# Performance work log

Measured on AMD Instinct MI355X. Metric: run time of the kernel, lower is better.

The kernel has to match this reference:

```python
import jax, jax.numpy as jnp
import numpy as np

BOHR = 1.8897261258369282  # Angstrom -> Bohr, as in SKparam
CUTOFF = 6.0
LATTICE = np.diag([5.0, 5.0, 5.0]).astype(np.float32)
N_ATOMS, N_SPECIES, N_POLY, N_KPT = 512, 4, 12, 32


def _compute_shifts():
    # Exact replica of DFTB.compute_shift in numpy.
    inv = np.linalg.inv(LATTICE)
    n_rep = np.ceil(np.linalg.norm(inv, axis=0) * CUTOFF).astype(int)
    grid = np.stack(np.meshgrid(*[np.arange(-n, n + 1) for n in n_rep], indexing='ij'), -1).reshape(-1, 3)
    a = np.where(grid > 0, grid - 1, grid)
    shrunk = np.where(a < 0, grid + 1, a)              # shrink each component toward 0 by 1
    sh2 = shrunk.astype(np.float32) @ LATTICE           # lattice.T @ r == r @ lattice
    keep = np.linalg.norm(sh2, axis=1) < CUTOFF
    return (grid[keep].astype(np.float32) @ LATTICE)    # [S,3], S=81 for this lattice/cutoff


def setup_inputs() -> dict:
    key = jax.random.key(0)
    k1, k2, k3, k4, k5 = jax.random.split(key, 5)
    positions = jax.random.uniform(k1, (N_ATOMS, 3), dtype=jnp.float32) * 5.0
    species = jax.random.randint(k2, (N_ATOMS,), 0, N_SPECIES)
    kpoints = jax.random.uniform(k3, (N_KPT, 3), dtype=jnp.float32)
    # decaying per-degree scale keeps polyval bounded at x = cutoff*BOHR ~ 11.3
    scale = (1.0 / 12.0) ** jnp.arange(N_POLY, dtype=jnp.float32)
    param_matrix = jax.random.normal(k4, (N_SPECIES, N_SPECIES, N_POLY), dtype=jnp.float32) * scale
    onsite = jax.random.normal(k5, (N_SPECIES,), dtype=jnp.float32)
    shifts = jnp.asarray(_compute_shifts())
    return {"positions": positions, "species": species, "kpoints": kpoints,
            "param_matrix": param_matrix, "onsite": onsite, "shifts": shifts}


def reference(positions, species, kpoints, param_matrix, onsite, shifts):
    # pairwise distance vectors under periodic shifts: [N,N,S,3]
    dvec = positions[None, :, None, :] + shifts[None, None, :, :] - positions[:, :, None][:, None].reshape(-1, 1, 1, 3)
    dvec = positions[None, :, None, :] + shifts[None, None, :, :] - positions[:, None, None, :]
    dr2 = jnp.sum(dvec * dvec, axis=-1)                       # [N,N,S]
    dr = jnp.sqrt(jnp.where(dr2 > 0.0, dr2, 1.0))
    dr = jnp.where(dr2 > 0.0, dr, 0.0)
    x = dr * BOHR
    # species-pair gather of Vsss polynomial coefficients: [N,N,P]
    coeffs = param_matrix[species[:, None], species[None, :]]
    # Horner eval (torch polyval: p[0] is the constant term after fliplr)
    y = jnp.zeros_like(x)
    for k in range(N_POLY - 1, -1, -1):
        y = y * x + coeffs[:, :, k][:, :, None]
    # calc_tb_params mask: zero for onsite (dr<=0.1) and beyond cutoff
    V = jnp.where((dr > 0.1) & (dr <= CUTOFF), y, 0.0)        # [N,N,S]
    # Bloch phases per k-point and shift (calc_phase_matrix, vectorized)
    inv_lat = jnp.asarray(np.linalg.inv(LATTICE))
    kc = kpoints @ inv_lat.T                                   # [K,3]
    ang = (2.0 * np.pi) * (kc @ shifts.T)                      # [K,S]
    Hr = jnp.einsum('ijs,ks->kij', V, jnp.cos(ang))            # [K,N,N]
    Hi = jnp.einsum('ijs,ks->kij', V, jnp.sin(ang))
    Hr = Hr + jnp.diag(onsite[species])[None]                  # onsite diagonal
    return jnp.stack([Hr, Hi])                                 # [2,K,N,N] real view of complex H
```

## Files before the change

### kernel.cpp

```cpp
#include <hip/hip_runtime.h>

#define NATOMS 512
#define NKPT 32
#define NPOLY 12
#define NSMAX 96
#define NSP 4
#define TI 4
#define TJ 64
#define NTHREADS 256

__global__ __launch_bounds__(NTHREADS, 4)
void dftb_kernel(const float* __restrict__ positions,
                 const int* __restrict__ species,
                 const float* __restrict__ kpoints,
                 const float* __restrict__ param,
                 const float* __restrict__ onsite,
                 const float* __restrict__ shifts,
                 float* __restrict__ out,
                 int ns)
{
    __shared__ float tab[NSMAX][64];
    __shared__ float4 sh4[NSMAX];
    __shared__ float cpar[NSP*NSP*NPOLY];
    __shared__ float4 pjs[TJ];
    __shared__ float4 pis[TI];
    __shared__ int sjs[TJ];
    __shared__ int sis[TI];

    const int tid = threadIdx.x;
    const int bi = blockIdx.x >> 3;
    const int bj = blockIdx.x & 7;

    if (ns > NSMAX) ns = NSMAX;

    for (int idx = tid; idx < ns; idx += NTHREADS)
        sh4[idx] = make_float4(shifts[idx*3+0], shifts[idx*3+1], shifts[idx*3+2], 0.0f);
    for (int idx = tid; idx < NSP*NSP*NPOLY; idx += NTHREADS)
        cpar[idx] = param[idx];
    if (tid < TJ) {
        int j = bj*TJ + tid;
        pjs[tid] = make_float4(positions[j*3+0], positions[j*3+1], positions[j*3+2], 0.0f);
        sjs[tid] = species[j];
    } else if (tid < TJ + TI) {
        int r = tid - TJ;
        int i = bi*TI + r;
        pis[r] = make_float4(positions[i*3+0], positions[i*3+1], positions[i*3+2], 0.0f);
        sis[r] = species[i];
    }
    for (int idx = tid; idx < ns*NKPT; idx += NTHREADS) {
        int s = idx >> 5;
        int k = idx & 31;
        float kcx = kpoints[k*3+0] * 0.2f;
        float kcy = kpoints[k*3+1] * 0.2f;
        float kcz = kpoints[k*3+2] * 0.2f;
        float d = (kcx*shifts[s*3+0] + kcy*shifts[s*3+1]) + kcz*shifts[s*3+2];
        float ang = 6.283185307179586f * d;
        float sn, cs;
        sincosf(ang, &sn, &cs);
        tab[s][k]      = cs;
        tab[s][32 + k] = sn;
    }
    __syncthreads();

    const int li = tid >> 6;
    const int lj = tid & 63;
    const int i = bi*TI + li;
    const int j = bj*TJ + lj;
    const float4 pi4 = pis[li];
    const float4 pj4 = pjs[lj];
    const int si = sis[li];
    const int sj = sjs[lj];

    float c[NPOLY];
    #pragma unroll
    for (int q = 0; q < NPOLY; ++q) c[q] = cpar[(si*NSP + sj)*NPOLY + q];

    float accR[NKPT], accI[NKPT];
    #pragma unroll
    for (int k = 0; k < NKPT; ++k) { accR[k] = 0.0f; accI[k] = 0.0f; }

    for (int s = 0; s < ns; ++s) {
        const float4 sh = sh4[s];
        float dx = (pj4.x + sh.x) - pi4.x;
        float dy = (pj4.y + sh.y) - pi4.y;
        float dz = (pj4.z + sh.z) - pi4.z;
        float dr2 = (__fmul_rn(dx,dx) + __fmul_rn(dy,dy)) + __fmul_rn(dz,dz);
        float dr = sqrtf(dr2);
        bool ok = (dr > 0.1f) && (dr <= 6.0f);
        if (__ballot(ok) == 0ULL) continue;
        float x = dr * 1.8897261258369282f;
        float y = c[NPOLY-1];
        #pragma unroll
        for (int q = NPOLY-2; q >= 0; --q) y = fmaf(y, x, c[q]);
        float V = ok ? y : 0.0f;
        const float4* tp = (const float4*)(&tab[s][0]);
        #pragma unroll
        for (int q = 0; q < 8; ++q) {
            float4 cv = tp[q];
            accR[4*q+0] = fmaf(V, cv.x, accR[4*q+0]);
            accR[4*q+1] = fmaf(V, cv.y, accR[4*q+1]);
            accR[4*q+2] = fmaf(V, cv.z, accR[4*q+2]);
            accR[4*q+3] = fmaf(V, cv.w, accR[4*q+3]);
        }
        #pragma unroll
        for (int q = 0; q < 8; ++q) {
            float4 sv = tp[8+q];
            accI[4*q+0] = fmaf(V, sv.x, accI[4*q+0]);
            accI[4*q+1] = fmaf(V, sv.y, accI[4*q+1]);
            accI[4*q+2] = fmaf(V, sv.z, accI[4*q+2]);
            accI[4*q+3] = fmaf(V, sv.w, accI[4*q+3]);
        }
    }

    const float oi = (i == j) ? onsite[si] : 0.0f;
    float* outR = out + (size_t)i*NATOMS + j;
    float* outI = outR + (size_t)NKPT*NATOMS*NATOMS;
    #pragma unroll
    for (int k = 0; k < NKPT; ++k) {
        outR[(size_t)k*NATOMS*NATOMS] = accR[k] + oi;
        outI[(size_t)k*NATOMS*NATOMS] = accI[k];
    }
}

extern "C" void kernel_launch(void* const* d_in, const int* in_sizes, int n_in,
                              void* d_out, int out_size, void* d_ws, size_t ws_size,
                              hipStream_t stream) {
    const float* positions = (const float*)d_in[0];
    const int*   species   = (const int*)d_in[1];
    const float* kpoints   = (const float*)d_in[2];
    const float* param     = (const float*)d_in[3];
    const float* onsite    = (const float*)d_in[4];
    const float* shifts    = (const float*)d_in[5];
    int ns = in_sizes[5] / 3;
    float* out = (float*)d_out;

    dim3 grid((NATOMS/TI) * (NATOMS/TJ));
    dftb_kernel<<<grid, NTHREADS, 0, stream>>>(positions, species, kpoints,
                                               param, onsite, shifts, out, ns);
}
```

Before: 40.66 us.

## Compute shift-phase contraction with bf16 MFMA via shared-memory V and phase tiles

Restructures the kernel into two phases. First, each thread evaluates the masked polynomial V for all shifts and stores it as bf16 in shared memory, alongside a bf16 cos/sin phase table. Then each wave runs 16x16x32 bf16 MFMA instructions to contract V against the phase table, writing float4 rows per k-point with onsite added on the diagonal. This moves the dominant FMA contraction off the vector ALUs onto matrix cores, at the cost of bf16 rounding of V and the phases and of larger shared-memory use that lowers occupancy.

```diff
diff --git a/kernel.cpp b/kernel.cpp
--- a/kernel.cpp
+++ b/kernel.cpp
@@ -1,124 +1,135 @@
 #include <hip/hip_runtime.h>
 
 #define NATOMS 512
+#define N2 (NATOMS*NATOMS)
 #define NKPT 32
 #define NPOLY 12
+#define NSP 4
 #define NSMAX 96
-#define NSP 4
+#define KSTR 104
 #define TI 4
 #define TJ 64
 #define NTHREADS 256
 
-__global__ __launch_bounds__(NTHREADS, 4)
-void dftb_kernel(const float* __restrict__ positions,
-                 const int* __restrict__ species,
-                 const float* __restrict__ kpoints,
-                 const float* __restrict__ param,
-                 const float* __restrict__ onsite,
-                 const float* __restrict__ shifts,
-                 float* __restrict__ out,
-                 int ns)
+typedef __attribute__((ext_vector_type(8))) short bf16x8;
+typedef __attribute__((ext_vector_type(4))) float f32x4;
+
+static __device__ __forceinline__ unsigned short f2bf(float f) {
+    union { float f; unsigned u; } x; x.f = f;
+    unsigned r = x.u + 0x7FFFu + ((x.u >> 16) & 1u);
+    return (unsigned short)(r >> 16);
+}
+
+__global__ __launch_bounds__(NTHREADS, 2)
+void dftb_mfma(const float* __restrict__ positions,
+               const int* __restrict__ species,
+               const float* __restrict__ kpoints,
+               const float* __restrict__ param,
+               const float* __restrict__ onsite,
+               const float* __restrict__ shifts,
+               float* __restrict__ out, int ns)
 {
-    __shared__ float tab[NSMAX][64];
+    __shared__ unsigned short Vt[NTHREADS][KSTR];
+    __shared__ unsigned short Tt[64][KSTR];
     __shared__ float4 sh4[NSMAX];
     __shared__ float cpar[NSP*NSP*NPOLY];
-    __shared__ float4 pjs[TJ];
-    __shared__ float4 pis[TI];
-    __shared__ int sjs[TJ];
-    __shared__ int sis[TI];
 
     const int tid = threadIdx.x;
     const int bi = blockIdx.x >> 3;
     const int bj = blockIdx.x & 7;
-
     if (ns > NSMAX) ns = NSMAX;
 
-    for (int idx = tid; idx < ns; idx += NTHREADS)
-        sh4[idx] = make_float4(shifts[idx*3+0], shifts[idx*3+1], shifts[idx*3+2], 0.0f);
+    for (int idx = tid; idx < 64*(KSTR/2); idx += NTHREADS)
+        ((unsigned*)Tt)[idx] = 0u;
+    for (int idx = tid; idx < NSMAX; idx += NTHREADS) {
+        if (idx < ns) sh4[idx] = make_float4(shifts[idx*3], shifts[idx*3+1], shifts[idx*3+2], 0.f);
+        else          sh4[idx] = make_float4(0.f, 0.f, 0.f, 0.f);
+    }
     for (int idx = tid; idx < NSP*NSP*NPOLY; idx += NTHREADS)
         cpar[idx] = param[idx];
-    if (tid < TJ) {
-        int j = bj*TJ + tid;
-        pjs[tid] = make_float4(positions[j*3+0], positions[j*3+1], positions[j*3+2], 0.0f);
-        sjs[tid] = species[j];
-    } else if (tid < TJ + TI) {
-        int r = tid - TJ;
-        int i = bi*TI + r;
-        pis[r] = make_float4(positions[i*3+0], positions[i*3+1], positions[i*3+2], 0.0f);
-        sis[r] = species[i];
+    __syncthreads();
+
+    for (int idx = tid; idx < ns*NKPT; idx += NTHREADS) {
+        int s = idx >> 5, k = idx & 31;
+        float4 sh = sh4[s];
+        float d = (kpoints[k*3]*0.2f*sh.x + kpoints[k*3+1]*0.2f*sh.y) + kpoints[k*3+2]*0.2f*sh.z;
+        float sn, cs;
+        sincosf(6.283185307179586f * d, &sn, &cs);
+        Tt[k][s]      = f2bf(cs);
+        Tt[k+32][s]   = f2bf(sn);
     }
-    for (int idx = tid; idx < ns*NKPT; idx += NTHREADS) {
-        int s = idx >> 5;
-        int k = idx & 31;
-        float kcx = kpoints[k*3+0] * 0.2f;
-        float kcy = kpoints[k*3+1] * 0.2f;
-        float kcz = kpoints[k*3+2] * 0.2f;
-        float d = (kcx*shifts[s*3+0] + kcy*shifts[s*3+1]) + kcz*shifts[s*3+2];
-        float ang = 6.283185307179586f * d;
-        float sn, cs;
-        sincosf(ang, &sn, &cs);
-        tab[s][k]      = cs;
-        tab[s][32 + k] = sn;
+
+    {
+        const int li = tid >> 6, lj = tid & 63;
+        const int i = bi*TI + li, j = bj*TJ + lj;
+        const float pix = positions[i*3], piy = positions[i*3+1], piz = positions[i*3+2];
+        const float pjx = positions[j*3], pjy = positions[j*3+1], pjz = positions[j*3+2];
+        const int si = species[i], sj = species[j];
+        float c[NPOLY];
+        #pragma unroll
+        for (int q = 0; q < NPOLY; ++q) c[q] = cpar[(si*NSP + sj)*NPOLY + q];
+        unsigned* vrow = (unsigned*)&Vt[tid][0];
+        for (int s2 = 0; s2 < NSMAX/2; ++s2) {
+            float v01[2] = {0.f, 0.f};
+            #pragma unroll
+            for (int h = 0; h < 2; ++h) {
+                int s = 2*s2 + h;
+                if (s < ns) {
+                    float4 sh = sh4[s];
+                    float dx = (pjx + sh.x) - pix;
+                    float dy = (pjy + sh.y) - piy;
+                    float dz = (pjz + sh.z) - piz;
+                    float dr2 = (__fmul_rn(dx,dx) + __fmul_rn(dy,dy)) + __fmul_rn(dz,dz);
+                    float dr = sqrtf(dr2);
+                    bool ok = (dr > 0.1f) && (dr <= 6.0f);
+                    if (__ballot(ok) != 0ULL) {
+                        float x = dr * 1.8897261258369282f;
+                        float y = c[NPOLY-1];
+                        #pragma unroll
+                        for (int q = NPOLY-2; q >= 0; --q) y = fmaf(y, x, c[q]);
+                        v01[h] = ok ? y : 0.f;
+                    }
+                }
+            }
+            vrow[s2] = (unsigned)f2bf(v01[0]) | ((unsigned)f2bf(v01[1]) << 16);
+        }
     }
     __syncthreads();
 
-    const int li = tid >> 6;
-    const int lj = tid & 63;
-    const int i = bi*TI + li;
-    const int j = bj*TJ + lj;
-    const float4 pi4 = pis[li];
-    const float4 pj4 = pjs[lj];
-    const int si = sis[li];
-    const int sj = sjs[lj];
+    const int w = tid >> 6, lane = tid & 63;
+    const int r16 = lane & 15, g = lane >> 4;
 
-    float c[NPOLY];
+    bf16x8 Bf[4][3];
     #pragma unroll
-    for (int q = 0; q < NPOLY; ++q) c[q] = cpar[(si*NSP + sj)*NPOLY + q];
+    for (int nf = 0; nf < 4; ++nf)
+        #pragma unroll
+        for (int kf = 0; kf < 3; ++kf)
+            Bf[nf][kf] = *(const bf16x8*)&Tt[nf*16 + r16][kf*32 + g*8];
 
-    float accR[NKPT], accI[NKPT];
+    const int irow = bi*TI + w;
+    const float ons = onsite[species[irow]];
+
     #pragma unroll
-    for (int k = 0; k < NKPT; ++k) { accR[k] = 0.0f; accI[k] = 0.0f; }
-
-    for (int s = 0; s < ns; ++s) {
-        const float4 sh = sh4[s];
-        float dx = (pj4.x + sh.x) - pi4.x;
-        float dy = (pj4.y + sh.y) - pi4.y;
-        float dz = (pj4.z + sh.z) - pi4.z;
-        float dr2 = (__fmul_rn(dx,dx) + __fmul_rn(dy,dy)) + __fmul_rn(dz,dz);
-        float dr = sqrtf(dr2);
-        bool ok = (dr > 0.1f) && (dr <= 6.0f);
-        if (__ballot(ok) == 0ULL) continue;
-        float x = dr * 1.8897261258369282f;
-        float y = c[NPOLY-1];
+    for (int mf = 0; mf < 4; ++mf) {
+        const int arow = w*64 + mf*16 + r16;
+        bf16x8 A0 = *(const bf16x8*)&Vt[arow][      g*8];
+        bf16x8 A1 = *(const bf16x8*)&Vt[arow][32 +  g*8];
+        bf16x8 A2 = *(const bf16x8*)&Vt[arow][64 +  g*8];
         #pragma unroll
-        for (int q = NPOLY-2; q >= 0; --q) y = fmaf(y, x, c[q]);
-        float V = ok ? y : 0.0f;
-        const float4* tp = (const float4*)(&tab[s][0]);
-        #pragma unroll
-        for (int q = 0; q < 8; ++q) {
-            float4 cv = tp[q];
-            accR[4*q+0] = fmaf(V, cv.x, accR[4*q+0]);
-            accR[4*q+1] = fmaf(V, cv.y, accR[4*q+1]);
-            accR[4*q+2] = fmaf(V, cv.z, accR[4*q+2]);
-            accR[4*q+3] = fmaf(V, cv.w, accR[4*q+3]);
+        for (int nf = 0; nf < 4; ++nf) {
+            f32x4 acc = {0.f, 0.f, 0.f, 0.f};
+            acc = __builtin_amdgcn_mfma_f32_16x16x32_bf16(A0, Bf[nf][0], acc, 0, 0, 0);
+            acc = __builtin_amdgcn_mfma_f32_16x16x32_bf16(A1, Bf[nf][1], acc, 0, 0, 0);
+            acc = __builtin_amdgcn_mfma_f32_16x16x32_bf16(A2, Bf[nf][2], acc, 0, 0, 0);
+            const int kcol = nf*16 + r16;
+            const int jb   = bj*TJ + mf*16 + g*4;
+            float4 v; v.x = acc[0]; v.y = acc[1]; v.z = acc[2]; v.w = acc[3];
+            if (kcol < 32) {
+                int q = irow - jb;
+                if (q >= 0 && q < 4) ((float*)&v)[q] += ons;
+            }
+            *(float4*)(out + (size_t)kcol*N2 + (size_t)irow*NATOMS + jb) = v;
         }
-        #pragma unroll
-        for (int q = 0; q < 8; ++q) {
-            float4 sv = tp[8+q];
-            accI[4*q+0] = fmaf(V, sv.x, accI[4*q+0]);
-            accI[4*q+1] = fmaf(V, sv.y, accI[4*q+1]);
-            accI[4*q+2] = fmaf(V, sv.z, accI[4*q+2]);
-            accI[4*q+3] = fmaf(V, sv.w, accI[4*q+3]);
-        }
-    }
-
-    const float oi = (i == j) ? onsite[si] : 0.0f;
-    float* outR = out + (size_t)i*NATOMS + j;
-    float* outI = outR + (size_t)NKPT*NATOMS*NATOMS;
-    #pragma unroll
-    for (int k = 0; k < NKPT; ++k) {
-        outR[(size_t)k*NATOMS*NATOMS] = accR[k] + oi;
-        outI[(size_t)k*NATOMS*NATOMS] = accI[k];
     }
 }
 
@@ -135,6 +146,6 @@
     float* out = (float*)d_out;
 
     dim3 grid((NATOMS/TI) * (NATOMS/TJ));
-    dftb_kernel<<<grid, NTHREADS, 0, stream>>>(positions, species, kpoints,
-                                               param, onsite, shifts, out, ns);
+    dftb_mfma<<<grid, NTHREADS, 0, stream>>>(positions, species, kpoints,
+                                             param, onsite, shifts, out, ns);
 }
```

Result: slower. 73.37 us (+80.4%).
